# Kernel optimization log

Hardware: AMD Instinct MI355X
Metric: run time of the kernel (lower is better)

Reference implementation:

```python
import jax, jax.numpy as jnp
import numpy as np

N_NODES = 100000
N_EDGES = 3200000
IN_FEAT = 512
HID = 32
N_CLASSES = 10


def gcn_conv(x, W, b, src, dst, num_nodes):
    """PyG GCNConv: linear transform, then symmetric-normalized aggregation
    with self-loops. out_i = sum_{j->i} norm_ij * (x_j W) + d_i^{-1} * (x_i W) + b."""
    h = x @ W  # [N, out]
    ones = jnp.ones(src.shape[0], dtype=x.dtype)
    deg = jax.ops.segment_sum(ones, dst, num_segments=num_nodes) + 1.0  # +1 self-loop
    dinv = jax.lax.rsqrt(deg)
    norm = dinv[src] * dinv[dst]  # [E]
    msg = h[src] * norm[:, None]  # [E, out]
    agg = jax.ops.segment_sum(msg, dst, num_segments=num_nodes)
    agg = agg + h * (dinv * dinv)[:, None]  # self-loop term (norm = d^-1)
    return agg + b


def setup_inputs() -> dict:
    key = jax.random.key(0)
    ks = jax.random.split(key, 12)
    x0 = jax.random.normal(ks[0], (N_NODES, IN_FEAT), dtype=jnp.float32)
    edge_index = jax.random.randint(ks[1], (2, N_EDGES), 0, N_NODES, dtype=jnp.int64)
    batch = jnp.zeros((N_NODES,), dtype=jnp.int64)

    def glorot(k, shape):
        fan_in, fan_out = shape
        lim = jnp.sqrt(6.0 / (fan_in + fan_out)).astype(jnp.float32)
        return jax.random.uniform(k, shape, jnp.float32, -lim, lim)

    return {
        "x0": x0,
        "edge_index": edge_index,
        "batch": batch,
        "W1": glorot(ks[2], (IN_FEAT, HID)),
        "b1": jnp.zeros((HID,), jnp.float32),
        "W2": glorot(ks[3], (HID, HID)),
        "b2": jnp.zeros((HID,), jnp.float32),
        "W3": glorot(ks[4], (HID, HID)),
        "b3": jnp.zeros((HID,), jnp.float32),
        "lin1_W": glorot(ks[5], (HID, 16)),
        "lin1_b": jnp.zeros((16,), jnp.float32),
        "lin2_W": glorot(ks[6], (16, N_CLASSES)),
        "lin2_b": jnp.zeros((N_CLASSES,), jnp.float32),
    }


def reference(x0, edge_index, batch, W1, b1, W2, b2, W3, b3,
              lin1_W, lin1_b, lin2_W, lin2_b):
    src, dst = edge_index[0], edge_index[1]
    n = x0.shape[0]
    x1 = jax.nn.relu(gcn_conv(x0, W1, b1, src, dst, n))
    x2 = jax.nn.relu(gcn_conv(x1, W2, b2, src, dst, n))
    x3 = jax.nn.relu(gcn_conv(x2, W3, b3, src, dst, n))
    # NOTE: original code computes cat([x1,x2,x3]) but then uses only x3; we match that.
    x = jax.nn.relu(x3 @ lin1_W + lin1_b)
    # dropout p=0.5 is identity in eval mode
    x = x @ lin2_W + lin2_b
    return x
```

## Files before the change

### kernel.cpp

```cpp
#include <hip/hip_runtime.h>
#include <hip/hip_bf16.h>

typedef float f32x4 __attribute__((ext_vector_type(4)));

#define N_NODES 100000
#define NBUK 391
#define BSHIFT 8
#define HBLK 256

__global__ void k_detect(const int* __restrict__ ei, int* __restrict__ mode) {
    __shared__ int flag;
    if (threadIdx.x == 0) flag = 0;
    __syncthreads();
    int f = 0;
    for (int i = threadIdx.x; i < 4096; i += 256)
        if (ei[2 * i + 1] != 0) f = 1;
    if (f) flag = 1;
    __syncthreads();
    if (threadIdx.x == 0) *mode = flag;
}

__global__ __launch_bounds__(256) void k_hist(const int* __restrict__ ei,
                                              const int* __restrict__ mode,
                                              int* __restrict__ gh, int E, int chunk) {
    __shared__ int hist[NBUK];
    int tid = threadIdx.x, k = blockIdx.x;
    for (int b = tid; b < NBUK; b += 256) hist[b] = 0;
    __syncthreads();
    int m = *mode;
    int e0 = k * chunk, e1 = min(E, e0 + chunk);
    for (int e = e0 + tid; e < e1; e += 256) {
        int d = m ? ei[E + e] : ei[2 * (E + e)];
        if ((unsigned)d >= N_NODES) d = 0;
        atomicAdd(&hist[d >> BSHIFT], 1);
    }
    __syncthreads();
    for (int b = tid; b < NBUK; b += 256) gh[k * NBUK + b] = hist[b];
}

__global__ __launch_bounds__(256) void k_btot(const int* __restrict__ gh, int* __restrict__ btot) {
    __shared__ int s[256];
    int b = blockIdx.x, tid = threadIdx.x;
    s[tid] = gh[tid * NBUK + b];
    __syncthreads();
    for (int d = 128; d > 0; d >>= 1) {
        if (tid < d) s[tid] += s[tid + d];
        __syncthreads();
    }
    if (tid == 0) btot[b] = s[0];
}

__global__ void k_scan_btot(const int* __restrict__ btot, int* __restrict__ bbase,
                            int* __restrict__ rowptr, int E) {
    __shared__ int s[512];
    int tid = threadIdx.x;
    int v = (tid < NBUK) ? btot[tid] : 0;
    s[tid] = v;
    __syncthreads();
    for (int d = 1; d < 512; d <<= 1) {
        int t = (tid >= d) ? s[tid - d] : 0;
        __syncthreads();
        s[tid] += t;
        __syncthreads();
    }
    if (tid < NBUK) bbase[tid] = s[tid] - v;
    if (tid == 0) { bbase[NBUK] = E; rowptr[N_NODES] = E; }
}

__global__ __launch_bounds__(256) void k_scan_cols(int* __restrict__ gh, const int* __restrict__ bbase) {
    __shared__ int s[256];
    int b = blockIdx.x, tid = threadIdx.x;
    int v = gh[tid * NBUK + b];
    s[tid] = v;
    __syncthreads();
    for (int d = 1; d < 256; d <<= 1) {
        int t = (tid >= d) ? s[tid - d] : 0;
        __syncthreads();
        s[tid] += t;
        __syncthreads();
    }
    gh[tid * NBUK + b] = bbase[b] + s[tid] - v;
}

__global__ __launch_bounds__(256) void k_bucketize(const int* __restrict__ ei,
                                                   const int* __restrict__ mode,
                                                   const int* __restrict__ offs,
                                                   int2* __restrict__ bp, int E, int chunk) {
    __shared__ int cur[NBUK];
    int tid = threadIdx.x, k = blockIdx.x;
    for (int b = tid; b < NBUK; b += 256) cur[b] = offs[k * NBUK + b];
    __syncthreads();
    int m = *mode;
    int e0 = k * chunk, e1 = min(E, e0 + chunk);
    for (int e = e0 + tid; e < e1; e += 256) {
        int s, d;
        if (m) { s = ei[e]; d = ei[E + e]; }
        else   { s = ei[2 * e]; d = ei[2 * (E + e)]; }
        if ((unsigned)s >= N_NODES) s = 0;
        if ((unsigned)d >= N_NODES) d = 0;
        int pos = atomicAdd(&cur[d >> BSHIFT], 1);
        int2 p; p.x = s; p.y = d;
        bp[pos] = p;
    }
}

__global__ __launch_bounds__(256) void k_build_csr(const int2* __restrict__ bp,
                                                   const int* __restrict__ bbase,
                                                   int* __restrict__ rowptr,
                                                   float* __restrict__ dinv,
                                                   int* __restrict__ csr) {
    __shared__ int cnt[256];
    __shared__ int s[256];
    __shared__ int cur[256];
    int b = blockIdx.x, tid = threadIdx.x;
    int nb = b << BSHIFT;
    int estart = bbase[b], eend = bbase[b + 1];
    cnt[tid] = 0;
    __syncthreads();
    for (int e = estart + tid; e < eend; e += 256) {
        int2 p = bp[e];
        atomicAdd(&cnt[p.y - nb], 1);
    }
    __syncthreads();
    int v = cnt[tid];
    s[tid] = v;
    __syncthreads();
    for (int d = 1; d < 256; d <<= 1) {
        int t = (tid >= d) ? s[tid - d] : 0;
        __syncthreads();
        s[tid] += t;
        __syncthreads();
    }
    int excl = s[tid] - v;
    int node = nb + tid;
    if (node < N_NODES) {
        rowptr[node] = estart + excl;
        dinv[node] = rsqrtf((float)v + 1.0f);
    }
    cur[tid] = estart + excl;
    __syncthreads();
    for (int e = estart + tid; e < eend; e += 256) {
        int2 p = bp[e];
        int pos = atomicAdd(&cur[p.y - nb], 1);
        csr[pos] = p.x;
    }
}

#define G1_KC 16
#define G1_ROWS 256
__global__ __launch_bounds__(256) void k_gemm1(const float* __restrict__ X,
                                               const float* __restrict__ W,
                                               const float* __restrict__ dinv,
                                               float* __restrict__ H) {
    __shared__ float xs[G1_ROWS * 20];
    int tid = threadIdx.x;
    long row0 = (long)blockIdx.x * G1_ROWS;
    long myrow = row0 + tid;

    float acc[32];
#pragma unroll
    for (int c = 0; c < 32; c++) acc[c] = 0.f;

    for (int k0 = 0; k0 < 512; k0 += G1_KC) {
        __syncthreads();
#pragma unroll
        for (int u = 0; u < 4; u++) {
            int idx = u * 256 + tid;
            int rr = idx >> 2, j = idx & 3;
            long grow = row0 + rr;
            f32x4 v = {0.f, 0.f, 0.f, 0.f};
            if (grow < N_NODES) v = *(const f32x4*)&X[grow * 512 + k0 + 4 * j];
            *(f32x4*)&xs[rr * 20 + 4 * j] = v;
        }
        __syncthreads();
#pragma unroll
        for (int kk = 0; kk < G1_KC; kk += 4) {
            f32x4 xq = *(const f32x4*)&xs[tid * 20 + kk];
            const float* wbase = &W[(long)(k0 + kk) * 32];
#pragma unroll
            for (int q = 0; q < 4; q++) {
                float xk = xq[q];
#pragma unroll
                for (int c = 0; c < 32; c++)
                    acc[c] = fmaf(xk, wbase[q * 32 + c], acc[c]);
            }
        }
    }
    if (myrow < N_NODES) {
        float dv = dinv[myrow];
        float* out = &H[myrow * 32];
#pragma unroll
        for (int c = 0; c < 32; c += 4) {
            f32x4 v;
            v.x = acc[c] * dv; v.y = acc[c + 1] * dv;
            v.z = acc[c + 2] * dv; v.w = acc[c + 3] * dv;
            *(f32x4*)&out[c] = v;
        }
    }
}

__device__ __forceinline__ float gather_sum(const float* __restrict__ Hf,
                                            const int* __restrict__ csr,
                                            int e0, int e1, int f) {
    float a0 = 0.f, a1 = 0.f, a2 = 0.f, a3 = 0.f;
    for (int base = e0; base < e1; base += 32) {
        int idx = base + f;
        int sl = (idx < e1) ? csr[idx] : 0;
        int mm = e1 - base;
        if (mm >= 32) {
#pragma unroll
            for (int j = 0; j < 32; j += 4) {
                int s0 = __shfl(sl, j, 32);
                int s1 = __shfl(sl, j + 1, 32);
                int s2 = __shfl(sl, j + 2, 32);
                int s3 = __shfl(sl, j + 3, 32);
                a0 += Hf[(long)s0 * 32];
                a1 += Hf[(long)s1 * 32];
                a2 += Hf[(long)s2 * 32];
                a3 += Hf[(long)s3 * 32];
            }
        } else {
            for (int j = 0; j < mm; j++) {
                int s0 = __shfl(sl, j, 32);
                a0 += Hf[(long)s0 * 32];
            }
        }
    }
    return (a0 + a1) + (a2 + a3);
}

__global__ __launch_bounds__(256) void k_agg_mm(const float* __restrict__ H,
                                                const int* __restrict__ rowptr,
                                                const int* __restrict__ csr,
                                                const float* __restrict__ dinv,
                                                const float* __restrict__ bias,
                                                const float* __restrict__ W,
                                                float* __restrict__ Hout, int n) {
    __shared__ float ws[1024];
    int tid = threadIdx.x;
    for (int t = tid; t < 1024; t += 256) ws[t] = W[t];
    __syncthreads();
    int node = blockIdx.x * 8 + (tid >> 5);
    int f = tid & 31;
    if (node >= n) return;
    int e0 = rowptr[node], e1 = rowptr[node + 1];
    const float* Hf = H + f;
    float asum = gather_sum(Hf, csr, e0, e1, f);
    float dv = dinv[node];
    float v = dv * (asum + Hf[(long)node * 32]) + bias[f];
    v = fmaxf(v, 0.f);
    float o = 0.f;
#pragma unroll
    for (int k = 0; k < 32; k++) {
        float vk = __shfl(v, k, 32);
        o += vk * ws[k * 32 + f];
    }
    Hout[(long)node * 32 + f] = o * dv;
}

__global__ __launch_bounds__(256) void k_agg_head(const float* __restrict__ H,
                                                  const int* __restrict__ rowptr,
                                                  const int* __restrict__ csr,
                                                  const float* __restrict__ dinv,
                                                  const float* __restrict__ bias,
                                                  const float* __restrict__ L1W,
                                                  const float* __restrict__ L1B,
                                                  const float* __restrict__ L2W,
                                                  const float* __restrict__ L2B,
                                                  float* __restrict__ out, int n) {
    __shared__ float w1[512];
    __shared__ float w2[160];
    __shared__ float bb1[16];
    __shared__ float bb2[10];
    int tid = threadIdx.x;
    for (int t = tid; t < 512; t += 256) w1[t] = L1W[t];
    if (tid < 160) w2[tid] = L2W[tid];
    if (tid < 16) bb1[tid] = L1B[tid];
    if (tid < 10) bb2[tid] = L2B[tid];
    __syncthreads();
    int node = blockIdx.x * 8 + (tid >> 5);
    int f = tid & 31;
    if (node >= n) return;
    int e0 = rowptr[node], e1 = rowptr[node + 1];
    const float* Hf = H + f;
    float asum = gather_sum(Hf, csr, e0, e1, f);
    float dv = dinv[node];
    float v = dv * (asum + Hf[(long)node * 32]) + bias[f];
    v = fmaxf(v, 0.f);
    int c1 = f & 15;
    float t1 = 0.f;
#pragma unroll
    for (int k = 0; k < 32; k++) {
        float vk = __shfl(v, k, 32);
        t1 += vk * w1[k * 16 + c1];
    }
    t1 = fmaxf(t1 + bb1[c1], 0.f);
    int c2 = (f < 10) ? f : 0;
    float o = 0.f;
#pragma unroll
    for (int k = 0; k < 16; k++) {
        float tk = __shfl(t1, k, 32);
        o += tk * w2[k * 10 + c2];
    }
    o += bb2[c2];
    if (f < 10) out[(long)node * 10 + f] = o;
}

extern "C" void kernel_launch(void* const* d_in, const int* in_sizes, int n_in,
                              void* d_out, int out_size, void* d_ws, size_t ws_size,
                              hipStream_t stream) {
    const float* x0 = (const float*)d_in[0];
    const int* ei = (const int*)d_in[1];
    const float* W1 = (const float*)d_in[3];
    const float* b1 = (const float*)d_in[4];
    const float* W2 = (const float*)d_in[5];
    const float* b2 = (const float*)d_in[6];
    const float* W3 = (const float*)d_in[7];
    const float* b3 = (const float*)d_in[8];
    const float* l1W = (const float*)d_in[9];
    const float* l1b = (const float*)d_in[10];
    const float* l2W = (const float*)d_in[11];
    const float* l2b = (const float*)d_in[12];

    const int E = in_sizes[1] / 2;
    const int N = N_NODES;

    char* w = (char*)d_ws;
    float* h      = (float*)(w);
    float* xb     = (float*)(w + 12800000);
    int2*  bp     = (int2*) (w);
    int*   gh     = (int*)  (w + 25600000);
    int*   btot   = (int*)  (w + 26000384);
    int*   bbase  = (int*)  (w + 26001948);
    int*   rowptr = (int*)  (w + 26003516);
    float* dinv   = (float*)(w + 26403532);
    int*   csr    = (int*)  (w + 26803532);
    int*   mode   = (int*)  (w + 39603532);

    const int chunk = (E + HBLK - 1) / HBLK;
    const int AGB = (N + 7) / 8;
    const int G1B = (N + G1_ROWS - 1) / G1_ROWS;

    k_detect<<<1, 256, 0, stream>>>(ei, mode);
    k_hist<<<HBLK, 256, 0, stream>>>(ei, mode, gh, E, chunk);
    k_btot<<<NBUK, 256, 0, stream>>>(gh, btot);
    k_scan_btot<<<1, 512, 0, stream>>>(btot, bbase, rowptr, E);
    k_scan_cols<<<NBUK, 256, 0, stream>>>(gh, bbase);
    k_bucketize<<<HBLK, 256, 0, stream>>>(ei, mode, gh, bp, E, chunk);
    k_build_csr<<<NBUK, 256, 0, stream>>>(bp, bbase, rowptr, dinv, csr);

    k_gemm1<<<G1B, 256, 0, stream>>>(x0, W1, dinv, h);
    k_agg_mm<<<AGB, 256, 0, stream>>>(h, rowptr, csr, dinv, b1, W2, xb, N);
    k_agg_mm<<<AGB, 256, 0, stream>>>(xb, rowptr, csr, dinv, b2, W3, h, N);
    k_agg_head<<<AGB, 256, 0, stream>>>(h, rowptr, csr, dinv, b3,
                                        l1W, l1b, l2W, l2b, (float*)d_out, N);
}
```

Before: 869.7 us.

## Compute first-layer GEMM with split-bf16 MFMA instead of scalar FP32 FMAs

Replaces the LDS-tiled scalar FP32 GEMM for x0@W1 with a wave-level MFMA 16x16x32 bf16 kernel. Both X and W are split into hi and lo bf16 parts, and three MFMA products (hh, lh, hl) approximate FP32 accuracy. A new prep kernel packs W1 into the MFMA operand layout. This removes the compute bottleneck of the 100000x512x32 GEMM, leaving it bound by reading X. The cost is some precision and extra conversion work per element. The Bh/Bl buffers reuse the gh workspace region, which is safe only if gh is dead by the time k_prepw runs.

```diff
diff --git a/kernel.cpp b/kernel.cpp
--- a/kernel.cpp
+++ b/kernel.cpp
@@ -2,6 +2,7 @@
 #include <hip/hip_bf16.h>
 
 typedef float f32x4 __attribute__((ext_vector_type(4)));
+typedef short bf16x8 __attribute__((ext_vector_type(8)));
 
 #define N_NODES 100000
 #define NBUK 391
@@ -146,56 +147,84 @@
     }
 }
 
-#define G1_KC 16
-#define G1_ROWS 256
+__device__ __forceinline__ unsigned short f2bf(float x) {
+    unsigned u = __float_as_uint(x);
+    unsigned lsb = (u >> 16) & 1;
+    u += 0x7fffu + lsb;
+    return (unsigned short)(u >> 16);
+}
+__device__ __forceinline__ float bf2f(unsigned short h) {
+    return __uint_as_float(((unsigned)h) << 16);
+}
+
+__global__ __launch_bounds__(256) void k_prepw(const float* __restrict__ W,
+                                               unsigned* __restrict__ Bh,
+                                               unsigned* __restrict__ Bl) {
+    int idx = blockIdx.x * 256 + threadIdx.x;
+    if (idx >= 8192) return;
+    int dw = idx & 3, lane = (idx >> 2) & 63, ct = (idx >> 8) & 1, kc = idx >> 9;
+    int c = lane & 15, kg = lane >> 4;
+    int col = ct * 16 + c;
+    unsigned h01 = 0, l01 = 0;
+#pragma unroll
+    for (int e = 0; e < 2; e++) {
+        int k = kc * 32 + kg * 8 + dw * 2 + e;
+        float w = W[k * 32 + col];
+        unsigned short wh = f2bf(w);
+        unsigned short wl = f2bf(w - bf2f(wh));
+        h01 |= ((unsigned)wh) << (16 * e);
+        l01 |= ((unsigned)wl) << (16 * e);
+    }
+    Bh[idx] = h01;
+    Bl[idx] = l01;
+}
+
 __global__ __launch_bounds__(256) void k_gemm1(const float* __restrict__ X,
-                                               const float* __restrict__ W,
+                                               const unsigned* __restrict__ Bh,
+                                               const unsigned* __restrict__ Bl,
                                                const float* __restrict__ dinv,
                                                float* __restrict__ H) {
-    __shared__ float xs[G1_ROWS * 20];
     int tid = threadIdx.x;
-    long row0 = (long)blockIdx.x * G1_ROWS;
-    long myrow = row0 + tid;
-
-    float acc[32];
-#pragma unroll
-    for (int c = 0; c < 32; c++) acc[c] = 0.f;
-
-    for (int k0 = 0; k0 < 512; k0 += G1_KC) {
-        __syncthreads();
-#pragma unroll
-        for (int u = 0; u < 4; u++) {
-            int idx = u * 256 + tid;
-            int rr = idx >> 2, j = idx & 3;
-            long grow = row0 + rr;
-            f32x4 v = {0.f, 0.f, 0.f, 0.f};
-            if (grow < N_NODES) v = *(const f32x4*)&X[grow * 512 + k0 + 4 * j];
-            *(f32x4*)&xs[rr * 20 + 4 * j] = v;
+    int lane = tid & 63;
+    int wv = tid >> 6;
+    long r0 = (long)blockIdx.x * 64 + wv * 16;
+    if (r0 >= N_NODES) return;
+    int row = lane & 15, kg = lane >> 4;
+    const float* xrow = X + (r0 + row) * 512 + kg * 8;
+
+    f32x4 acc0 = {0.f, 0.f, 0.f, 0.f};
+    f32x4 acc1 = {0.f, 0.f, 0.f, 0.f};
+
+    for (int kc = 0; kc < 16; kc++) {
+        f32x4 xa = *(const f32x4*)(xrow + kc * 32);
+        f32x4 xb = *(const f32x4*)(xrow + kc * 32 + 4);
+        float xv[8] = {xa.x, xa.y, xa.z, xa.w, xb.x, xb.y, xb.z, xb.w};
+        bf16x8 ah, al;
+#pragma unroll
+        for (int i = 0; i < 8; i++) {
+            unsigned short h = f2bf(xv[i]);
+            ah[i] = (short)h;
+            al[i] = (short)f2bf(xv[i] - bf2f(h));
         }
-        __syncthreads();
-#pragma unroll
-        for (int kk = 0; kk < G1_KC; kk += 4) {
-            f32x4 xq = *(const f32x4*)&xs[tid * 20 + kk];
-            const float* wbase = &W[(long)(k0 + kk) * 32];
-#pragma unroll
-            for (int q = 0; q < 4; q++) {
-                float xk = xq[q];
-#pragma unroll
-                for (int c = 0; c < 32; c++)
-                    acc[c] = fmaf(xk, wbase[q * 32 + c], acc[c]);
-            }
-        }
-    }
-    if (myrow < N_NODES) {
-        float dv = dinv[myrow];
-        float* out = &H[myrow * 32];
-#pragma unroll
-        for (int c = 0; c < 32; c += 4) {
-            f32x4 v;
-            v.x = acc[c] * dv; v.y = acc[c + 1] * dv;
-            v.z = acc[c + 2] * dv; v.w = acc[c + 3] * dv;
-            *(f32x4*)&out[c] = v;
-        }
+        const bf16x8 bh0 = *(const bf16x8*)(Bh + ((kc * 2 + 0) * 64 + lane) * 4);
+        const bf16x8 bh1 = *(const bf16x8*)(Bh + ((kc * 2 + 1) * 64 + lane) * 4);
+        const bf16x8 bl0 = *(const bf16x8*)(Bl + ((kc * 2 + 0) * 64 + lane) * 4);
+        const bf16x8 bl1 = *(const bf16x8*)(Bl + ((kc * 2 + 1) * 64 + lane) * 4);
+        acc0 = __builtin_amdgcn_mfma_f32_16x16x32_bf16(ah, bh0, acc0, 0, 0, 0);
+        acc1 = __builtin_amdgcn_mfma_f32_16x16x32_bf16(ah, bh1, acc1, 0, 0, 0);
+        acc0 = __builtin_amdgcn_mfma_f32_16x16x32_bf16(al, bh0, acc0, 0, 0, 0);
+        acc1 = __builtin_amdgcn_mfma_f32_16x16x32_bf16(al, bh1, acc1, 0, 0, 0);
+        acc0 = __builtin_amdgcn_mfma_f32_16x16x32_bf16(ah, bl0, acc0, 0, 0, 0);
+        acc1 = __builtin_amdgcn_mfma_f32_16x16x32_bf16(ah, bl1, acc1, 0, 0, 0);
+    }
+
+    int c = lane & 15;
+#pragma unroll
+    for (int j = 0; j < 4; j++) {
+        long grow = r0 + kg * 4 + j;
+        float dv = dinv[grow];
+        H[grow * 32 + c]      = acc0[j] * dv;
+        H[grow * 32 + 16 + c] = acc1[j] * dv;
     }
 }
 
@@ -330,6 +359,8 @@
     float* xb     = (float*)(w + 12800000);
     int2*  bp     = (int2*) (w);
     int*   gh     = (int*)  (w + 25600000);
+    unsigned* Bh  = (unsigned*)(w + 25600000);
+    unsigned* Bl  = (unsigned*)(w + 25632768);
     int*   btot   = (int*)  (w + 26000384);
     int*   bbase  = (int*)  (w + 26001948);
     int*   rowptr = (int*)  (w + 26003516);
@@ -339,7 +370,7 @@
 
     const int chunk = (E + HBLK - 1) / HBLK;
     const int AGB = (N + 7) / 8;
-    const int G1B = (N + G1_ROWS - 1) / G1_ROWS;
+    const int G1B = (N + 63) / 64;
 
     k_detect<<<1, 256, 0, stream>>>(ei, mode);
     k_hist<<<HBLK, 256, 0, stream>>>(ei, mode, gh, E, chunk);
@@ -347,9 +378,10 @@
     k_scan_btot<<<1, 512, 0, stream>>>(btot, bbase, rowptr, E);
     k_scan_cols<<<NBUK, 256, 0, stream>>>(gh, bbase);
     k_bucketize<<<HBLK, 256, 0, stream>>>(ei, mode, gh, bp, E, chunk);
+    k_prepw<<<32, 256, 0, stream>>>(W1, Bh, Bl);
     k_build_csr<<<NBUK, 256, 0, stream>>>(bp, bbase, rowptr, dinv, csr);
 
-    k_gemm1<<<G1B, 256, 0, stream>>>(x0, W1, dinv, h);
+    k_gemm1<<<G1B, 256, 0, stream>>>(x0, Bh, Bl, dinv, h);
     k_agg_mm<<<AGB, 256, 0, stream>>>(h, rowptr, csr, dinv, b1, W2, xb, N);
     k_agg_mm<<<AGB, 256, 0, stream>>>(xb, rowptr, csr, dinv, b2, W3, h, N);
     k_agg_head<<<AGB, 256, 0, stream>>>(h, rowptr, csr, dinv, b3,
```

Result: faster. 762.7 us (-12.3%).
